# Kernel optimization log

Measured on AMD Instinct MI355X. Metric: run time of the kernel, lower is better.

## Reference

```python
import jax, jax.numpy as jnp
import numpy as np

NH = 12          # num_heads
EPS = 1e-6       # eps for LayerNorm and QK RMSNorm
THETA = 10000.0


def _layernorm(x):
    # WanLayerNorm: fp32 layer-norm, no affine
    x = x.astype(jnp.float32)
    m = x.mean(-1, keepdims=True)
    v = ((x - m) ** 2).mean(-1, keepdims=True)
    return (x - m) * jax.lax.rsqrt(v + EPS)


def _rmsnorm(x, g):
    # WanRMSNorm: fp32 rms-norm then scale by weight g
    x32 = x.astype(jnp.float32)
    return x32 * jax.lax.rsqrt((x32 * x32).mean(-1, keepdims=True) + EPS) * g


def _rope_cos_sin(T, H, W, head_dim):
    # Per-token 3D RoPE angle tables. head_dim=128 -> half=64 complex pairs,
    # split [22, 21, 21] across (T, H, W) axes, matching rope_params/_build_freqs.
    half = head_dim // 2
    p_t = half - 2 * (half // 3)
    p_h = half // 3
    p_w = half // 3

    def ang(L, h):
        inv = 1.0 / (THETA ** (np.arange(h, dtype=np.float64) / h))
        return np.outer(np.arange(L, dtype=np.float64), inv)  # [L, h]

    a_t = np.broadcast_to(ang(T, p_t)[:, None, None, :], (T, H, W, p_t))
    a_h = np.broadcast_to(ang(H, p_h)[None, :, None, :], (T, H, W, p_h))
    a_w = np.broadcast_to(ang(W, p_w)[None, None, :, :], (T, H, W, p_w))
    a = np.concatenate([a_t, a_h, a_w], axis=-1).reshape(T * H * W, half)
    return jnp.asarray(np.cos(a), jnp.float32), jnp.asarray(np.sin(a), jnp.float32)


def _rope_apply(x, cos, sin):
    # x: [B, S, n, d]; pairs are interleaved along last dim (view_as_complex of reshape(..., -1, 2))
    xr = x[..., 0::2]
    xi = x[..., 1::2]
    c = cos[None, :, None, :]
    s = sin[None, :, None, :]
    out_r = xr * c - xi * s
    out_i = xr * s + xi * c
    return jnp.stack([out_r, out_i], axis=-1).reshape(x.shape)


def setup_inputs() -> dict:
    key = jax.random.key(0)
    ks = jax.random.split(key, 8)
    B, C, T, H, W = 1, 1536, 8, 22, 22
    scale = 1.0 / np.sqrt(C)
    return {
        "x": jax.random.normal(ks[0], (B, C, T, H, W), jnp.float32),
        "Wq": jax.random.normal(ks[1], (C, C), jnp.float32) * scale,
        "bq": jnp.zeros((C,), jnp.float32),
        "Wk": jax.random.normal(ks[2], (C, C), jnp.float32) * scale,
        "bk": jnp.zeros((C,), jnp.float32),
        "Wv": jax.random.normal(ks[3], (C, C), jnp.float32) * scale,
        "bv": jnp.zeros((C,), jnp.float32),
        "Wo": jax.random.normal(ks[4], (C, C), jnp.float32) * scale,
        "bo": jnp.zeros((C,), jnp.float32),
        "gq": jnp.ones((C,), jnp.float32),
        "gk": jnp.ones((C,), jnp.float32),
    }


def reference(x, Wq, bq, Wk, bk, Wv, bv, Wo, bo, gq, gk):
    B, C, T, H, W = x.shape
    S = T * H * W
    n = NH
    d = C // n

    # [B, C, T, H, W] -> [B, S, C]
    x_in = jnp.transpose(x, (0, 2, 3, 4, 1)).reshape(B, S, C)
    xn = _layernorm(x_in)

    # QKV projections + QK RMSNorm
    q = _rmsnorm(xn @ Wq.T + bq, gq).reshape(B, S, n, d)
    k = _rmsnorm(xn @ Wk.T + bk, gk).reshape(B, S, n, d)
    v = (xn @ Wv.T + bv).reshape(B, S, n, d)

    # 3D RoPE on q, k
    cos, sin = _rope_cos_sin(T, H, W, d)
    q = _rope_apply(q, cos, sin)
    k = _rope_apply(k, cos, sin)

    # scaled dot-product attention (flash_attention with default 1/sqrt(d) scale)
    scale = 1.0 / jnp.sqrt(jnp.float32(d))
    logits = jnp.einsum("bqhd,bkhd->bhqk", q, k) * scale
    attn = jax.nn.softmax(logits, axis=-1)
    o = jnp.einsum("bhqk,bkhd->bqhd", attn, v).reshape(B, S, C)

    # output projection + residual
    y = x_in + (o @ Wo.T + bo)
    return jnp.transpose(y.reshape(B, T, H, W, C), (0, 4, 1, 2, 3))
```

## Files before the change

kernel.cpp:

```cpp
#include <hip/hip_runtime.h>

#define S_TOT 3872
#define C_DIM 1536
#define NHEAD 12
#define DHEAD 128
#define TT 8
#define HH 22
#define WW 22
#define NKT 61

typedef __bf16 bf16x8 __attribute__((ext_vector_type(8)));
typedef float  f32x4  __attribute__((ext_vector_type(4)));
typedef unsigned short u16x8 __attribute__((ext_vector_type(8)));

__device__ __forceinline__ float bf2f(unsigned short u) {
    unsigned int v = ((unsigned int)u) << 16;
    float f; __builtin_memcpy(&f, &v, 4); return f;
}
__device__ __forceinline__ unsigned short f2bf(float f) {
    unsigned int u; __builtin_memcpy(&u, &f, 4);
    u += 0x7fffu + ((u >> 16) & 1u);
    return (unsigned short)(u >> 16);
}
__device__ __forceinline__ unsigned int pk2_trunc(float a, float b) {
    unsigned int ua, ub;
    __builtin_memcpy(&ua, &a, 4); __builtin_memcpy(&ub, &b, 4);
    return (ua >> 16) | (ub & 0xffff0000u);
}
__device__ __forceinline__ float ldin(const void* p, size_t i, int isf32) {
    if (isf32) return ((const float*)p)[i];
    return bf2f(((const unsigned short*)p)[i]);
}
__device__ __forceinline__ float fexp2(float x) {
#if __has_builtin(__builtin_amdgcn_exp2f)
    return __builtin_amdgcn_exp2f(x);
#else
    return exp2f(x);
#endif
}
__device__ __forceinline__ void async16(const void* g, void* l) {
    __builtin_amdgcn_global_load_lds(
        (const __attribute__((address_space(1))) unsigned int*)g,
        (__attribute__((address_space(3))) unsigned int*)l, 16, 0, 0);
}
__device__ __forceinline__ int xcd_swz(int bid, int nwg) {
    int q = nwg >> 3, r = nwg & 7;
    int xcd = bid & 7, i = bid >> 3;
    int base = (xcd < r) ? xcd * (q + 1) : r * (q + 1) + (xcd - r) * q;
    return base + i;
}

__global__ void detect_vecs(const unsigned short* __restrict__ x,
                            const void* p0, const void* p1, const void* p2,
                            const void* p3, const void* p4, const void* p5,
                            int* __restrict__ flag, unsigned short* __restrict__ vecs,
                            float* __restrict__ sumb, float* __restrict__ sumsqb) {
    __shared__ int cnt;
    if (threadIdx.x == 0) cnt = 0;
    __syncthreads();
    int c = 0;
    for (int i = 0; i < 8; ++i) {
        unsigned short u = x[threadIdx.x * 8 + i];
        int e = (u >> 7) & 0xFF;
        if (e >= 112 && e <= 143) c++;
    }
    atomicAdd(&cnt, c);
    for (int j = threadIdx.x; j < S_TOT; j += 256) {
        sumb[j] = 0.f; sumsqb[j] = 0.f;
    }
    __syncthreads();
    int isf32 = (cnt >= 1900) ? 0 : 1;
    if (threadIdx.x == 0) *flag = isf32;
    const void* ps[6] = {p0, p1, p2, p3, p4, p5};
    for (int v = 0; v < 6; ++v)
        for (int j = threadIdx.x; j < C_DIM; j += 256)
            vecs[v * C_DIM + j] = f2bf(ldin(ps[v], j, isf32));
}

__global__ __launch_bounds__(256) void wconv4(const void* __restrict__ s0,
                                              const void* __restrict__ s1,
                                              const void* __restrict__ s2,
                                              const void* __restrict__ s3,
                                              const int* __restrict__ flag,
                                              unsigned short* __restrict__ d0,
                                              unsigned short* __restrict__ d1,
                                              unsigned short* __restrict__ d2,
                                              unsigned short* __restrict__ d3) {
    const void* srcs[4] = {s0, s1, s2, s3};
    unsigned short* dsts[4] = {d0, d1, d2, d3};
    const void* src = srcs[blockIdx.y];
    unsigned short* dst = dsts[blockIdx.y];
    size_t i = ((size_t)blockIdx.x * 256 + threadIdx.x) * 8;
    if (*flag) {
        const float* s = (const float*)src + i;
        float4 a = *(const float4*)s, b = *(const float4*)(s + 4);
        u16x8 o;
        o[0]=f2bf(a.x); o[1]=f2bf(a.y); o[2]=f2bf(a.z); o[3]=f2bf(a.w);
        o[4]=f2bf(b.x); o[5]=f2bf(b.y); o[6]=f2bf(b.z); o[7]=f2bf(b.w);
        *(u16x8*)(dst + i) = o;
    } else {
        *(u16x8*)(dst + i) = *(const u16x8*)((const unsigned short*)src + i);
    }
}

__global__ __launch_bounds__(256) void ln_stats(const void* __restrict__ x,
                                                const int* __restrict__ flag,
                                                float* __restrict__ sumb,
                                                float* __restrict__ sumsqb) {
    int isf32 = *flag;
    int sl = threadIdx.x & 63, cg = threadIdx.x >> 6;
    int s = blockIdx.x * 64 + sl;
    int cbase = blockIdx.y * 384;
    float sum = 0.f, sumsq = 0.f;
    if (s < S_TOT) {
        for (int c = cbase + cg; c < cbase + 384; c += 4) {
            float v = ldin(x, (size_t)c * S_TOT + s, isf32);
            sum += v; sumsq += v * v;
        }
    }
    __shared__ float r0[4][64], r1[4][64];
    r0[cg][sl] = sum; r1[cg][sl] = sumsq;
    __syncthreads();
    if (cg == 0 && s < S_TOT) {
        float st = r0[0][sl] + r0[1][sl] + r0[2][sl] + r0[3][sl];
        float sq = r1[0][sl] + r1[1][sl] + r1[2][sl] + r1[3][sl];
        atomicAdd(&sumb[s], st);
        atomicAdd(&sumsqb[s], sq);
    }
}

__global__ __launch_bounds__(256) void ln_norm_t(const void* __restrict__ x,
                                                 const int* __restrict__ flag,
                                                 const float* __restrict__ sumb,
                                                 const float* __restrict__ sumsqb,
                                                 unsigned short* __restrict__ xn) {
    int isf32 = *flag;
    __shared__ float tile[32][33];
    int s0 = blockIdx.x * 32, c0 = blockIdx.y * 32;
    int tx = threadIdx.x, ty = threadIdx.y;
    for (int r = 0; r < 4; ++r) {
        int cl = ty + 8 * r;
        tile[cl][tx] = ldin(x, (size_t)(c0 + cl) * S_TOT + (s0 + tx), isf32);
    }
    __syncthreads();
    for (int r = 0; r < 4; ++r) {
        int sl = ty + 8 * r;
        int s = s0 + sl, c = c0 + tx;
        float m = sumb[s] * (1.0f / C_DIM);
        float var = sumsqb[s] * (1.0f / C_DIM) - m * m;
        float rstd = rsqrtf(var + 1e-6f);
        xn[(size_t)s * C_DIM + c] = f2bf((tile[tx][sl] - m) * rstd);
    }
}

template<int BN>
__global__ __launch_bounds__(256, 3) void gemm2p(const unsigned short* __restrict__ A,
                                                 const unsigned short* __restrict__ W,
                                                 const unsigned short* __restrict__ bias,
                                                 unsigned short* __restrict__ D0,
                                                 unsigned short* __restrict__ D1,
                                                 unsigned short* __restrict__ DT,
                                                 int nsplit, int ntrans) {
    constexpr int NGRP = 8 + BN / 16;
    constexpr int GPW  = NGRP / 4;
    __shared__ __align__(16) unsigned short As[2][128 * 32];
    __shared__ __align__(16) unsigned short Bs[2][BN * 32];
    int nwg = gridDim.x * gridDim.y;
    int wg  = xcd_swz(blockIdx.y * gridDim.x + blockIdx.x, nwg);
    int m0 = (wg % gridDim.x) * 128, n0 = (wg / gridDim.x) * BN;
    int tid = threadIdx.x;
    int wave = tid >> 6, lane = tid & 63;
    int lm = lane & 15, lq = lane >> 4;
    int wr = wave >> 1, wc = wave & 1;
    int srow = lane >> 2, scol = (lane & 3) * 8;

    f32x4 acc[4][BN / 32];
    #pragma unroll
    for (int a = 0; a < 4; ++a)
        #pragma unroll
        for (int b = 0; b < BN / 32; ++b) acc[a][b] = (f32x4){0.f, 0.f, 0.f, 0.f};

    #pragma unroll
    for (int t = 0; t < GPW; ++t) {
        int g = wave * GPW + t;
        if (g < 8) {
            int am = m0 + g * 16 + srow; if (am > S_TOT - 1) am = S_TOT - 1;
            async16(A + (size_t)am * C_DIM + scol, (char*)As[0] + g * 1024);
        } else {
            int bn = n0 + (g - 8) * 16 + srow;
            async16(W + (size_t)bn * C_DIM + scol, (char*)Bs[0] + (g - 8) * 1024);
        }
    }
    int cur = 0;
    for (int k0 = 0; k0 < C_DIM; k0 += 32) {
        int kn = k0 + 32;
        if (kn < C_DIM) {
            #pragma unroll
            for (int t = 0; t < GPW; ++t) {
                int g = wave * GPW + t;
                if (g < 8) {
                    int am = m0 + g * 16 + srow; if (am > S_TOT - 1) am = S_TOT - 1;
                    async16(A + (size_t)am * C_DIM + kn + scol, (char*)As[cur ^ 1] + g * 1024);
                } else {
                    int bn = n0 + (g - 8) * 16 + srow;
                    async16(W + (size_t)bn * C_DIM + kn + scol, (char*)Bs[cur ^ 1] + (g - 8) * 1024);
                }
            }
            asm volatile("s_waitcnt vmcnt(%0)" :: "i"(GPW) : "memory");
        } else {
            asm volatile("s_waitcnt vmcnt(0)" ::: "memory");
        }
        __builtin_amdgcn_sched_barrier(0);
        __builtin_amdgcn_s_barrier();
        __builtin_amdgcn_sched_barrier(0);

        bf16x8 af[4], bf[BN / 32];
        #pragma unroll
        for (int mb = 0; mb < 4; ++mb)
            af[mb] = *(const bf16x8*)((const char*)As[cur] + (wr * 64 + mb * 16 + lm) * 64 + lq * 16);
        #pragma unroll
        for (int nb = 0; nb < BN / 32; ++nb)
            bf[nb] = *(const bf16x8*)((const char*)Bs[cur] + (wc * (BN / 2) + nb * 16 + lm) * 64 + lq * 16);
        #pragma unroll
        for (int mb = 0; mb < 4; ++mb)
            #pragma unroll
            for (int nb = 0; nb < BN / 32; ++nb)
                acc[mb][nb] = __builtin_amdgcn_mfma_f32_16x16x32_bf16(af[mb], bf[nb], acc[mb][nb], 0, 0, 0);

        __builtin_amdgcn_sched_barrier(0);
        __builtin_amdgcn_s_barrier();
        __builtin_amdgcn_sched_barrier(0);
        cur ^= 1;
    }

    #pragma unroll
    for (int mb = 0; mb < 4; ++mb) {
        #pragma unroll
        for (int nb = 0; nb < BN / 32; ++nb) {
            int gn = n0 + wc * (BN / 2) + nb * 16 + lm;
            float bv = bf2f(bias[gn]);
            if (gn >= ntrans) {
                int gm0 = m0 + wr * 64 + mb * 16 + lq * 4;
                if (gm0 < S_TOT) {
                    ushort4 pk;
                    pk.x = f2bf(acc[mb][nb][0] + bv);
                    pk.y = f2bf(acc[mb][nb][1] + bv);
                    pk.z = f2bf(acc[mb][nb][2] + bv);
                    pk.w = f2bf(acc[mb][nb][3] + bv);
                    *(ushort4*)(DT + (size_t)(gn - ntrans) * S_TOT + gm0) = pk;
                }
            } else {
                unsigned short* dst = (gn < nsplit) ? D0 : D1;
                int cn = (gn < nsplit) ? gn : gn - nsplit;
                #pragma unroll
                for (int r = 0; r < 4; ++r) {
                    int gm = m0 + wr * 64 + mb * 16 + lq * 4 + r;
                    if (gm < S_TOT) dst[(size_t)gm * C_DIM + cn] = f2bf(acc[mb][nb][r] + bv);
                }
            }
        }
    }
}

__global__ __launch_bounds__(256) void rope2(unsigned short* __restrict__ qbuf,
                                             unsigned short* __restrict__ kbuf,
                                             const unsigned short* __restrict__ gq,
                                             const unsigned short* __restrict__ gk,
                                             float qsc) {
    int s = blockIdx.x;
    unsigned short* row = (blockIdx.y ? kbuf : qbuf) + (size_t)s * C_DIM;
    const unsigned short* g = blockIdx.y ? gk : gq;
    float premul = blockIdx.y ? 1.0f : qsc;
    int tid = threadIdx.x;
    float ss = 0.f;
    for (int i = 0; i < 6; ++i) {
        float v = bf2f(row[tid + 256 * i]);
        ss += v * v;
    }
    for (int off = 32; off; off >>= 1) ss += __shfl_down(ss, off, 64);
    __shared__ float wsum[4];
    __shared__ float scale_sh;
    if ((tid & 63) == 0) wsum[tid >> 6] = ss;
    __syncthreads();
    if (tid == 0) {
        float tot = wsum[0] + wsum[1] + wsum[2] + wsum[3];
        scale_sh = rsqrtf(tot * (1.0f / C_DIM) + 1e-6f) * premul;
    }
    __syncthreads();
    float scale = scale_sh;

    int t  = s / (HH * WW);
    int rm = s % (HH * WW);
    int hh = rm / WW, ww = rm % WW;

    float e[3][2];
    int cols[3];
    for (int i = 0; i < 3; ++i) {
        int p = tid + 256 * i;
        int j = p & 63;
        int col0 = (p >> 6) * DHEAD + 2 * j;
        cols[i] = col0;
        float e0 = bf2f(row[col0])     * scale * bf2f(g[col0]);
        float e1 = bf2f(row[col0 + 1]) * scale * bf2f(g[col0 + 1]);
        float pos, fr;
        if (j < 22)       { pos = (float)t;  fr = (float)j        * (1.0f / 22.0f); }
        else if (j < 43)  { pos = (float)hh; fr = (float)(j - 22) * (1.0f / 21.0f); }
        else              { pos = (float)ww; fr = (float)(j - 43) * (1.0f / 21.0f); }
        float ang = pos * expf(fr * -9.210340371976184f);
        float c = cosf(ang), sn = sinf(ang);
        e[i][0] = e0 * c - e1 * sn;
        e[i][1] = e0 * sn + e1 * c;
    }
    for (int i = 0; i < 3; ++i) {
        row[cols[i]]     = f2bf(e[i][0]);
        row[cols[i] + 1] = f2bf(e[i][1]);
    }
}

__global__ __launch_bounds__(128, 2) void attn_mfma(const unsigned short* __restrict__ q,
                                                    const unsigned short* __restrict__ kp,
                                                    const unsigned short* __restrict__ vt,
                                                    unsigned short* __restrict__ o) {
    __shared__ __align__(16) unsigned char Ks[16384];
    __shared__ __align__(16) unsigned char Vs[16384];
    __shared__ __align__(16) unsigned char Ps[8192];

    int bid = xcd_swz(blockIdx.x, NHEAD * NKT);
    int h  = bid / NKT;
    int qt = bid % NKT;
    int q0 = qt * 64;
    int tid = threadIdx.x;
    int wave = tid >> 6, lane = tid & 63;
    int lm = lane & 15, lq = lane >> 4;

    bf16x8 qf[2][4];
    #pragma unroll
    for (int g = 0; g < 2; ++g) {
        int qr = q0 + wave * 32 + g * 16 + lm; if (qr >= S_TOT) qr = S_TOT - 1;
        const unsigned short* qptr = q + (size_t)qr * C_DIM + h * DHEAD + lq * 8;
        #pragma unroll
        for (int kc = 0; kc < 4; ++kc) qf[g][kc] = *(const bf16x8*)(qptr + kc * 32);
    }

    int krow = lane >> 4;
    int kcolA = ((lane & 15) ^ krow) * 8;
    int kcolB = ((lane & 15) ^ (4 + krow)) * 8;
    int vr8 = lane >> 3;
    int vslot = (lane & 7) ^ vr8;

    int sxor = (lm & 7) << 4;
    int ksoff[4], kqoff[4];
    #pragma unroll
    for (int nt = 0; nt < 4; ++nt) ksoff[nt] = (nt * 4 + (lm >> 2)) * 1024 + (lm & 3) * 256;
    #pragma unroll
    for (int kc = 0; kc < 4; ++kc) kqoff[kc] = (kc * 4 + lq) * 16;

    f32x4 oacc[2][8];
    #pragma unroll
    for (int g = 0; g < 2; ++g)
        #pragma unroll
        for (int i = 0; i < 8; ++i) oacc[g][i] = (f32x4){0.f, 0.f, 0.f, 0.f};
    float m_run[2] = {-__builtin_inff(), -__builtin_inff()};
    float l_run[2] = {0.f, 0.f};

    for (int kt = 0; kt < NKT; ++kt) {
        int k0 = kt * 64;
        #pragma unroll
        for (int t = 0; t < 8; ++t) {
            int g = wave * 8 + t;
            int grow = k0 + g * 4 + krow; if (grow > S_TOT - 1) grow = S_TOT - 1;
            async16(kp + (size_t)grow * C_DIM + h * DHEAD + ((g & 1) ? kcolB : kcolA),
                    Ks + g * 1024);
        }
        {
            int vcol = k0 + vslot * 8; if (vcol > S_TOT - 8) vcol = S_TOT - 8;
            #pragma unroll
            for (int t = 0; t < 8; ++t) {
                int g = wave * 8 + t;
                async16(vt + (size_t)(h * DHEAD + g * 8 + vr8) * S_TOT + vcol,
                        Vs + g * 1024);
            }
        }
        __syncthreads();

        f32x4 sacc[2][4];
        #pragma unroll
        for (int g = 0; g < 2; ++g)
            #pragma unroll
            for (int nt = 0; nt < 4; ++nt) sacc[g][nt] = (f32x4){0.f, 0.f, 0.f, 0.f};
        #pragma unroll
        for (int kc = 0; kc < 4; ++kc)
            #pragma unroll
            for (int nt = 0; nt < 4; ++nt) {
                bf16x8 kf = *(const bf16x8*)(Ks + ((ksoff[nt] + kqoff[kc]) ^ sxor));
                sacc[0][nt] = __builtin_amdgcn_mfma_f32_16x16x32_bf16(kf, qf[0][kc], sacc[0][nt], 0, 0, 0);
                sacc[1][nt] = __builtin_amdgcn_mfma_f32_16x16x32_bf16(kf, qf[1][kc], sacc[1][nt], 0, 0, 0);
            }
        if (kt == NKT - 1) {
            #pragma unroll
            for (int g = 0; g < 2; ++g)
                #pragma unroll
                for (int nt = 0; nt < 4; ++nt)
                    #pragma unroll
                    for (int r = 0; r < 4; ++r)
                        if (k0 + nt * 16 + lq * 4 + r >= S_TOT) sacc[g][nt][r] = -__builtin_inff();
        }
        #pragma unroll
        for (int g = 0; g < 2; ++g) {
            float mtr[4];
            #pragma unroll
            for (int nt = 0; nt < 4; ++nt)
                mtr[nt] = fmaxf(fmaxf(sacc[g][nt][0], sacc[g][nt][1]),
                                fmaxf(sacc[g][nt][2], sacc[g][nt][3]));
            float pmax = fmaxf(fmaxf(mtr[0], mtr[1]), fmaxf(mtr[2], mtr[3]));
            int defer = __all(pmax - m_run[g] <= 8.0f);
            if (!defer) {
                float rmax = fmaxf(pmax, __shfl_xor(pmax, 16, 64));
                rmax = fmaxf(rmax, __shfl_xor(rmax, 32, 64));
                float mn = fmaxf(m_run[g], rmax);
                float alpha = fexp2(m_run[g] - mn);
                l_run[g] *= alpha;
                #pragma unroll
                for (int i = 0; i < 8; ++i)
                    #pragma unroll
                    for (int r = 0; r < 4; ++r) oacc[g][i][r] *= alpha;
                m_run[g] = mn;
            }
            float rsn[4];
            #pragma unroll
            for (int nt = 0; nt < 4; ++nt) {
                float p0 = fexp2(sacc[g][nt][0] - m_run[g]);
                float p1 = fexp2(sacc[g][nt][1] - m_run[g]);
                float p2 = fexp2(sacc[g][nt][2] - m_run[g]);
                float p3 = fexp2(sacc[g][nt][3] - m_run[g]);
                sacc[g][nt][0] = p0; sacc[g][nt][1] = p1;
                sacc[g][nt][2] = p2; sacc[g][nt][3] = p3;
                rsn[nt] = (p0 + p1) + (p2 + p3);
            }
            l_run[g] += (rsn[0] + rsn[1]) + (rsn[2] + rsn[3]);
            #pragma unroll
            for (int nt = 0; nt < 4; ++nt) {
                uint2 pk;
                pk.x = pk2_trunc(sacc[g][nt][0], sacc[g][nt][1]);
                pk.y = pk2_trunc(sacc[g][nt][2], sacc[g][nt][3]);
                *(uint2*)(Ps + (wave * 4096 + g * 2048 + lm * 128 + ((nt * 32 + lq * 8) ^ sxor))) = pk;
            }
        }
        #pragma unroll
        for (int kc = 0; kc < 2; ++kc) {
            bf16x8 pf0 = *(const bf16x8*)(Ps + (wave * 4096 + lm * 128 + ((kc * 64 + lq * 16) ^ sxor)));
            bf16x8 pf1 = *(const bf16x8*)(Ps + (wave * 4096 + 2048 + lm * 128 + ((kc * 64 + lq * 16) ^ sxor)));
            #pragma unroll
            for (int mt = 0; mt < 8; ++mt) {
                bf16x8 vf = *(const bf16x8*)(Vs + ((mt * 16 + lm) * 128 + ((kc * 64 + lq * 16) ^ sxor)));
                oacc[0][mt] = __builtin_amdgcn_mfma_f32_16x16x32_bf16(vf, pf0, oacc[0][mt], 0, 0, 0);
                oacc[1][mt] = __builtin_amdgcn_mfma_f32_16x16x32_bf16(vf, pf1, oacc[1][mt], 0, 0, 0);
            }
        }
        __syncthreads();
    }
    #pragma unroll
    for (int g = 0; g < 2; ++g) {
        float lt = l_run[g];
        lt += __shfl_xor(lt, 16, 64);
        lt += __shfl_xor(lt, 32, 64);
        int qrow = q0 + wave * 32 + g * 16 + lm;
        if (qrow < S_TOT) {
            float inv = 1.0f / lt;
            #pragma unroll
            for (int mt = 0; mt < 8; ++mt) {
                ushort4 pk;
                pk.x = f2bf(oacc[g][mt][0] * inv);
                pk.y = f2bf(oacc[g][mt][1] * inv);
                pk.z = f2bf(oacc[g][mt][2] * inv);
                pk.w = f2bf(oacc[g][mt][3] * inv);
                *(ushort4*)(o + (size_t)qrow * C_DIM + h * DHEAD + mt * 16 + lq * 4) = pk;
            }
        }
    }
}

__global__ __launch_bounds__(256) void resid_t(const unsigned short* __restrict__ proj,
                                               const void* __restrict__ x,
                                               const int* __restrict__ flag,
                                               void* __restrict__ out) {
    int isf32 = *flag;
    __shared__ float tile[32][33];
    int s0 = blockIdx.x * 32, c0 = blockIdx.y * 32;
    int tx = threadIdx.x, ty = threadIdx.y;
    for (int r = 0; r < 4; ++r) {
        int sl = ty + 8 * r;
        tile[sl][tx] = bf2f(proj[(size_t)(s0 + sl) * C_DIM + (c0 + tx)]);
    }
    __syncthreads();
    for (int r = 0; r < 4; ++r) {
        int cl = ty + 8 * r;
        size_t idx = (size_t)(c0 + cl) * S_TOT + (s0 + tx);
        float val = ldin(x, idx, isf32) + tile[tx][cl];
        if (isf32) ((float*)out)[idx] = val;
        else       ((unsigned short*)out)[idx] = f2bf(val);
    }
}

extern "C" void kernel_launch(void* const* d_in, const int* in_sizes, int n_in,
                              void* d_out, int out_size, void* d_ws, size_t ws_size,
                              hipStream_t stream) {
    const void* x  = d_in[0];
    const void* Wq = d_in[1];
    const void* bq = d_in[2];
    const void* Wk = d_in[3];
    const void* bk = d_in[4];
    const void* Wv = d_in[5];
    const void* bv = d_in[6];
    const void* Wo = d_in[7];
    const void* bo = d_in[8];
    const void* gq = d_in[9];
    const void* gk = d_in[10];

    char* ws = (char*)d_ws;
    size_t off = 0;
    auto alloc = [&](size_t bytes) -> char* {
        char* p = ws + off;
        off += (bytes + 255) & ~(size_t)255;
        return p;
    };
    const size_t SC = (size_t)S_TOT * C_DIM;
    const size_t WSZ = (size_t)C_DIM * C_DIM * 2;
    unsigned short* xn   = (unsigned short*)alloc(SC * 2);
    unsigned short* qb   = (unsigned short*)alloc(SC * 2);
    unsigned short* kb   = (unsigned short*)alloc(SC * 2);
    unsigned short* Ws0  = (unsigned short*)alloc(WSZ);
    unsigned short* Ws1  = (unsigned short*)alloc(WSZ);
    unsigned short* Ws2  = (unsigned short*)alloc(WSZ);
    unsigned short* Ws3  = (unsigned short*)alloc(WSZ);
    unsigned short* vecs = (unsigned short*)alloc((size_t)6 * C_DIM * 2);
    float* sumb          = (float*)alloc((size_t)S_TOT * 4);
    float* sumsqb        = (float*)alloc((size_t)S_TOT * 4);
    int*   flag          = (int*)alloc(256);
    unsigned short* Vt   = (unsigned short*)d_out;
    unsigned short* ob   = xn;
    unsigned short* proj = qb;

    (void)Ws1; (void)Ws2;

    unsigned short* bo_b = vecs + 3 * C_DIM;
    unsigned short* gq_b = vecs + 4 * C_DIM;
    unsigned short* gk_b = vecs + 5 * C_DIM;

    const float QSC = 0.12751745f;

    dim3 t328(32, 8);
    dim3 tgrid(S_TOT / 32, C_DIM / 32);
    dim3 qkvgrid(31, 24);
    dim3 ogrid(31, 24);
    dim3 wgrid((C_DIM * C_DIM) / 2048, 4);
    dim3 sgrid(NKT, 4);
    dim3 rgrid(S_TOT, 2);

    detect_vecs<<<1, 256, 0, stream>>>((const unsigned short*)x, bq, bk, bv, bo, gq, gk,
                                       flag, vecs, sumb, sumsqb);
    wconv4<<<wgrid, 256, 0, stream>>>(Wq, Wk, Wv, Wo, flag, Ws0, Ws1, Ws2, Ws3);
    ln_stats<<<sgrid, 256, 0, stream>>>(x, flag, sumb, sumsqb);
    ln_norm_t<<<tgrid, t328, 0, stream>>>(x, flag, sumb, sumsqb, xn);

    gemm2p<192><<<qkvgrid, 256, 0, stream>>>(xn, Ws0, vecs, qb, kb, Vt, C_DIM, 2 * C_DIM);
    rope2<<<rgrid, 256, 0, stream>>>(qb, kb, gq_b, gk_b, QSC);

    attn_mfma<<<NHEAD * NKT, 128, 0, stream>>>(qb, kb, Vt, ob);

    gemm2p<64><<<ogrid, 256, 0, stream>>>(ob, Ws3, bo_b, proj, proj, proj, 1 << 30, 1 << 30);
    resid_t<<<tgrid, t328, 0, stream>>>(proj, x, flag, d_out);
}
```

Measured before the change: 469.9 us.

## Split attention KV range across two wave pairs and merge softmax partials

```diff
diff --git a/kernel.cpp b/kernel.cpp
--- a/kernel.cpp
+++ b/kernel.cpp
@@ -317,13 +317,13 @@
     }
 }
 
-__global__ __launch_bounds__(128, 2) void attn_mfma(const unsigned short* __restrict__ q,
+__global__ __launch_bounds__(256, 2) void attn_mfma(const unsigned short* __restrict__ q,
                                                     const unsigned short* __restrict__ kp,
                                                     const unsigned short* __restrict__ vt,
                                                     unsigned short* __restrict__ o) {
-    __shared__ __align__(16) unsigned char Ks[16384];
-    __shared__ __align__(16) unsigned char Vs[16384];
-    __shared__ __align__(16) unsigned char Ps[8192];
+    __shared__ __align__(16) unsigned char Ks[2][16384];
+    __shared__ __align__(16) unsigned char Vs[2][16384];
+    __shared__ __align__(16) unsigned char Ps[16384];
 
     int bid = xcd_swz(blockIdx.x, NHEAD * NKT);
     int h  = bid / NKT;
@@ -331,12 +331,16 @@
     int q0 = qt * 64;
     int tid = threadIdx.x;
     int wave = tid >> 6, lane = tid & 63;
+    int qw = wave & 1;
+    int kh = wave >> 1;
     int lm = lane & 15, lq = lane >> 4;
+    unsigned char* Ksh = Ks[kh];
+    unsigned char* Vsh = Vs[kh];
 
     bf16x8 qf[2][4];
     #pragma unroll
     for (int g = 0; g < 2; ++g) {
-        int qr = q0 + wave * 32 + g * 16 + lm; if (qr >= S_TOT) qr = S_TOT - 1;
+        int qr = q0 + qw * 32 + g * 16 + lm; if (qr >= S_TOT) qr = S_TOT - 1;
         const unsigned short* qptr = q + (size_t)qr * C_DIM + h * DHEAD + lq * 8;
         #pragma unroll
         for (int kc = 0; kc < 4; ++kc) qf[g][kc] = *(const bf16x8*)(qptr + kc * 32);
@@ -363,22 +367,25 @@
     float m_run[2] = {-__builtin_inff(), -__builtin_inff()};
     float l_run[2] = {0.f, 0.f};
 
-    for (int kt = 0; kt < NKT; ++kt) {
-        int k0 = kt * 64;
+    for (int it = 0; it < 31; ++it) {
+        int ktile = kh ? (31 + it) : it;
+        int dummy = (ktile > NKT - 1);
+        if (dummy) ktile = NKT - 1;
+        int k0 = ktile * 64;
         #pragma unroll
         for (int t = 0; t < 8; ++t) {
-            int g = wave * 8 + t;
+            int g = qw * 8 + t;
             int grow = k0 + g * 4 + krow; if (grow > S_TOT - 1) grow = S_TOT - 1;
             async16(kp + (size_t)grow * C_DIM + h * DHEAD + ((g & 1) ? kcolB : kcolA),
-                    Ks + g * 1024);
+                    Ksh + g * 1024);
         }
         {
             int vcol = k0 + vslot * 8; if (vcol > S_TOT - 8) vcol = S_TOT - 8;
             #pragma unroll
             for (int t = 0; t < 8; ++t) {
-                int g = wave * 8 + t;
+                int g = qw * 8 + t;
                 async16(vt + (size_t)(h * DHEAD + g * 8 + vr8) * S_TOT + vcol,
-                        Vs + g * 1024);
+                        Vsh + g * 1024);
             }
         }
         __syncthreads();
@@ -392,18 +399,19 @@
         for (int kc = 0; kc < 4; ++kc)
             #pragma unroll
             for (int nt = 0; nt < 4; ++nt) {
-                bf16x8 kf = *(const bf16x8*)(Ks + ((ksoff[nt] + kqoff[kc]) ^ sxor));
+                bf16x8 kf = *(const bf16x8*)(Ksh + ((ksoff[nt] + kqoff[kc]) ^ sxor));
                 sacc[0][nt] = __builtin_amdgcn_mfma_f32_16x16x32_bf16(kf, qf[0][kc], sacc[0][nt], 0, 0, 0);
                 sacc[1][nt] = __builtin_amdgcn_mfma_f32_16x16x32_bf16(kf, qf[1][kc], sacc[1][nt], 0, 0, 0);
             }
-        if (kt == NKT - 1) {
+        if (ktile == NKT - 1) {
             #pragma unroll
             for (int g = 0; g < 2; ++g)
                 #pragma unroll
                 for (int nt = 0; nt < 4; ++nt)
                     #pragma unroll
                     for (int r = 0; r < 4; ++r)
-                        if (k0 + nt * 16 + lq * 4 + r >= S_TOT) sacc[g][nt][r] = -__builtin_inff();
+                        if (dummy || (k0 + nt * 16 + lq * 4 + r >= S_TOT))
+                            sacc[g][nt][r] = -__builtin_inff();
         }
         #pragma unroll
         for (int g = 0; g < 2; ++g) {
@@ -452,29 +460,48 @@
             bf16x8 pf1 = *(const bf16x8*)(Ps + (wave * 4096 + 2048 + lm * 128 + ((kc * 64 + lq * 16) ^ sxor)));
             #pragma unroll
             for (int mt = 0; mt < 8; ++mt) {
-                bf16x8 vf = *(const bf16x8*)(Vs + ((mt * 16 + lm) * 128 + ((kc * 64 + lq * 16) ^ sxor)));
+                bf16x8 vf = *(const bf16x8*)(Vsh + ((mt * 16 + lm) * 128 + ((kc * 64 + lq * 16) ^ sxor)));
                 oacc[0][mt] = __builtin_amdgcn_mfma_f32_16x16x32_bf16(vf, pf0, oacc[0][mt], 0, 0, 0);
                 oacc[1][mt] = __builtin_amdgcn_mfma_f32_16x16x32_bf16(vf, pf1, oacc[1][mt], 0, 0, 0);
             }
         }
         __syncthreads();
     }
-    #pragma unroll
-    for (int g = 0; g < 2; ++g) {
-        float lt = l_run[g];
-        lt += __shfl_xor(lt, 16, 64);
-        lt += __shfl_xor(lt, 32, 64);
-        int qrow = q0 + wave * 32 + g * 16 + lm;
-        if (qrow < S_TOT) {
-            float inv = 1.0f / lt;
-            #pragma unroll
-            for (int mt = 0; mt < 8; ++mt) {
-                ushort4 pk;
-                pk.x = f2bf(oacc[g][mt][0] * inv);
-                pk.y = f2bf(oacc[g][mt][1] * inv);
-                pk.z = f2bf(oacc[g][mt][2] * inv);
-                pk.w = f2bf(oacc[g][mt][3] * inv);
-                *(ushort4*)(o + (size_t)qrow * C_DIM + h * DHEAD + mt * 16 + lq * 4) = pk;
+
+    float* mrg = (float*)Ks;
+    float* base = mrg + (qw * 64 + lane) * 68;
+    if (kh == 1) {
+        #pragma unroll
+        for (int g = 0; g < 2; ++g)
+            #pragma unroll
+            for (int mt = 0; mt < 8; ++mt)
+                *(f32x4*)(base + (g * 8 + mt) * 4) = oacc[g][mt];
+        base[64] = m_run[0]; base[65] = m_run[1];
+        base[66] = l_run[0]; base[67] = l_run[1];
+    }
+    __syncthreads();
+    if (kh == 0) {
+        #pragma unroll
+        for (int g = 0; g < 2; ++g) {
+            float m2 = base[64 + g], l2 = base[66 + g];
+            float mm = fmaxf(m_run[g], m2);
+            float a1 = fexp2(m_run[g] - mm), a2 = fexp2(m2 - mm);
+            float L = l_run[g] * a1 + l2 * a2;
+            L += __shfl_xor(L, 16, 64);
+            L += __shfl_xor(L, 32, 64);
+            int qrow = q0 + qw * 32 + g * 16 + lm;
+            if (qrow < S_TOT) {
+                float inv = 1.0f / L;
+                #pragma unroll
+                for (int mt = 0; mt < 8; ++mt) {
+                    f32x4 o2 = *(const f32x4*)(base + (g * 8 + mt) * 4);
+                    ushort4 pk;
+                    pk.x = f2bf((oacc[g][mt][0] * a1 + o2[0] * a2) * inv);
+                    pk.y = f2bf((oacc[g][mt][1] * a1 + o2[1] * a2) * inv);
+                    pk.z = f2bf((oacc[g][mt][2] * a1 + o2[2] * a2) * inv);
+                    pk.w = f2bf((oacc[g][mt][3] * a1 + o2[3] * a2) * inv);
+                    *(ushort4*)(o + (size_t)qrow * C_DIM + h * DHEAD + mt * 16 + lq * 4) = pk;
+                }
             }
         }
     }
@@ -566,7 +593,7 @@
     gemm2p<192><<<qkvgrid, 256, 0, stream>>>(xn, Ws0, vecs, qb, kb, Vt, C_DIM, 2 * C_DIM);
     rope2<<<rgrid, 256, 0, stream>>>(qb, kb, gq_b, gk_b, QSC);
 
-    attn_mfma<<<NHEAD * NKT, 128, 0, stream>>>(qb, kb, Vt, ob);
+    attn_mfma<<<NHEAD * NKT, 256, 0, stream>>>(qb, kb, Vt, ob);
 
     gemm2p<64><<<ogrid, 256, 0, stream>>>(ob, Ws3, bo_b, proj, proj, proj, 1 << 30, 1 << 30);
     resid_t<<<tgrid, t328, 0, stream>>>(proj, x, flag, d_out);
```

Result: no change. 473.2 us (+0.7%).

## Use three-stage LDS pipeline in GEMMs with one barrier per k-step

Applied to the files above, without the earlier changes.

```diff
diff --git a/kernel.cpp b/kernel.cpp
--- a/kernel.cpp
+++ b/kernel.cpp
@@ -154,7 +154,7 @@
 }
 
 template<int BN>
-__global__ __launch_bounds__(256, 3) void gemm2p(const unsigned short* __restrict__ A,
+__global__ __launch_bounds__(256, 3) void gemm3s(const unsigned short* __restrict__ A,
                                                  const unsigned short* __restrict__ W,
                                                  const unsigned short* __restrict__ bias,
                                                  unsigned short* __restrict__ D0,
@@ -163,8 +163,9 @@
                                                  int nsplit, int ntrans) {
     constexpr int NGRP = 8 + BN / 16;
     constexpr int GPW  = NGRP / 4;
-    __shared__ __align__(16) unsigned short As[2][128 * 32];
-    __shared__ __align__(16) unsigned short Bs[2][BN * 32];
+    constexpr int NSTEPS = C_DIM / 32;
+    __shared__ __align__(16) unsigned short As[3][128 * 32];
+    __shared__ __align__(16) unsigned short Bs[3][BN * 32];
     int nwg = gridDim.x * gridDim.y;
     int wg  = xcd_swz(blockIdx.y * gridDim.x + blockIdx.x, nwg);
     int m0 = (wg % gridDim.x) * 128, n0 = (wg / gridDim.x) * BN;
@@ -180,40 +181,34 @@
         #pragma unroll
         for (int b = 0; b < BN / 32; ++b) acc[a][b] = (f32x4){0.f, 0.f, 0.f, 0.f};
 
-    #pragma unroll
-    for (int t = 0; t < GPW; ++t) {
-        int g = wave * GPW + t;
-        if (g < 8) {
-            int am = m0 + g * 16 + srow; if (am > S_TOT - 1) am = S_TOT - 1;
-            async16(A + (size_t)am * C_DIM + scol, (char*)As[0] + g * 1024);
-        } else {
-            int bn = n0 + (g - 8) * 16 + srow;
-            async16(W + (size_t)bn * C_DIM + scol, (char*)Bs[0] + (g - 8) * 1024);
-        }
-    }
+#define G_STAGE(BUF, K0S) do {                                              \
+        _Pragma("unroll")                                                   \
+        for (int t_ = 0; t_ < GPW; ++t_) {                                  \
+            int g_ = wave * GPW + t_;                                       \
+            if (g_ < 8) {                                                   \
+                int am = m0 + g_ * 16 + srow; if (am > S_TOT - 1) am = S_TOT - 1; \
+                async16(A + (size_t)am * C_DIM + (K0S) + scol, (char*)As[BUF] + g_ * 1024); \
+            } else {                                                        \
+                int bn = n0 + (g_ - 8) * 16 + srow;                         \
+                async16(W + (size_t)bn * C_DIM + (K0S) + scol, (char*)Bs[BUF] + (g_ - 8) * 1024); \
+            }                                                               \
+        } } while (0)
+
+    G_STAGE(0, 0);
+    G_STAGE(1, 32);
     int cur = 0;
-    for (int k0 = 0; k0 < C_DIM; k0 += 32) {
-        int kn = k0 + 32;
-        if (kn < C_DIM) {
-            #pragma unroll
-            for (int t = 0; t < GPW; ++t) {
-                int g = wave * GPW + t;
-                if (g < 8) {
-                    int am = m0 + g * 16 + srow; if (am > S_TOT - 1) am = S_TOT - 1;
-                    async16(A + (size_t)am * C_DIM + kn + scol, (char*)As[cur ^ 1] + g * 1024);
-                } else {
-                    int bn = n0 + (g - 8) * 16 + srow;
-                    async16(W + (size_t)bn * C_DIM + kn + scol, (char*)Bs[cur ^ 1] + (g - 8) * 1024);
-                }
-            }
+    for (int t = 0; t < NSTEPS; ++t) {
+        if (t + 1 < NSTEPS)
             asm volatile("s_waitcnt vmcnt(%0)" :: "i"(GPW) : "memory");
-        } else {
+        else
             asm volatile("s_waitcnt vmcnt(0)" ::: "memory");
-        }
         __builtin_amdgcn_sched_barrier(0);
         __builtin_amdgcn_s_barrier();
         __builtin_amdgcn_sched_barrier(0);
 
+        int nxt = cur + 2; if (nxt >= 3) nxt -= 3;
+        if (t + 2 < NSTEPS) G_STAGE(nxt, (t + 2) * 32);
+
         bf16x8 af[4], bf[BN / 32];
         #pragma unroll
         for (int mb = 0; mb < 4; ++mb)
@@ -227,11 +222,9 @@
             for (int nb = 0; nb < BN / 32; ++nb)
                 acc[mb][nb] = __builtin_amdgcn_mfma_f32_16x16x32_bf16(af[mb], bf[nb], acc[mb][nb], 0, 0, 0);
 
-        __builtin_amdgcn_sched_barrier(0);
-        __builtin_amdgcn_s_barrier();
-        __builtin_amdgcn_sched_barrier(0);
-        cur ^= 1;
-    }
+        cur = cur + 1; if (cur >= 3) cur -= 3;
+    }
+#undef G_STAGE
 
     #pragma unroll
     for (int mb = 0; mb < 4; ++mb) {
@@ -551,7 +544,7 @@
 
     dim3 t328(32, 8);
     dim3 tgrid(S_TOT / 32, C_DIM / 32);
-    dim3 qkvgrid(31, 24);
+    dim3 qkvgrid(31, 36);
     dim3 ogrid(31, 24);
     dim3 wgrid((C_DIM * C_DIM) / 2048, 4);
     dim3 sgrid(NKT, 4);
@@ -563,11 +556,11 @@
     ln_stats<<<sgrid, 256, 0, stream>>>(x, flag, sumb, sumsqb);
     ln_norm_t<<<tgrid, t328, 0, stream>>>(x, flag, sumb, sumsqb, xn);
 
-    gemm2p<192><<<qkvgrid, 256, 0, stream>>>(xn, Ws0, vecs, qb, kb, Vt, C_DIM, 2 * C_DIM);
+    gemm3s<128><<<qkvgrid, 256, 0, stream>>>(xn, Ws0, vecs, qb, kb, Vt, C_DIM, 2 * C_DIM);
     rope2<<<rgrid, 256, 0, stream>>>(qb, kb, gq_b, gk_b, QSC);
 
     attn_mfma<<<NHEAD * NKT, 128, 0, stream>>>(qb, kb, Vt, ob);
 
-    gemm2p<64><<<ogrid, 256, 0, stream>>>(ob, Ws3, bo_b, proj, proj, proj, 1 << 30, 1 << 30);
+    gemm3s<64><<<ogrid, 256, 0, stream>>>(ob, Ws3, bo_b, proj, proj, proj, 1 << 30, 1 << 30);
     resid_t<<<tgrid, t328, 0, stream>>>(proj, x, flag, d_out);
 }
```

After: 489.7 us. +4.2%, slower.
